# Kernel tuning notes

Hardware: AMD Instinct MI355X
Metric: run time of the kernel (lower is better)

## Reference

```python
import jax, jax.numpy as jnp
import numpy as np

S = 3      # SAMPLE_SIZE
U = 4      # UPSCALE
HID = 64


def _forward(x_in, sampler_w, sampler_b, w1, b1, w2, b2, w3, b3, w4, b4, w5, b5, w6, b6):
    B, C, H, W = x_in.shape  # C == 1
    Hp, Wp = H - (S - 1), W - (S - 1)
    # unfold: every 3x3 patch -> flattened vector of 9 (row-major i*3+j), matches F.unfold ordering
    img = x_in[:, 0]  # [B,H,W]
    patches = jnp.stack(
        [img[:, i:i + Hp, j:j + Wp] for i in range(S) for j in range(S)], axis=-1
    )  # [B,Hp,Wp,9]
    # AutoSample: softmax over the 9 taps per output channel, bias forced to zero
    wsamp = jax.nn.softmax(sampler_w.reshape(4, S * S), axis=1)  # [4,9]
    s = jnp.einsum('bhwk,ck->bhwc', patches, wsamp) + sampler_b * 0.0  # [B,Hp,Wp,4]
    # PixelShuffle(2) on [N,4,1,1] -> [N,1,2,2]: spatial (i,j) = channel i*2+j.
    # conv1 (2x2 kernel on 2x2 input) == dense over those 4 values; w1 is conv1.weight.reshape(64,4)
    x = jnp.einsum('bhwc,oc->bhwo', s, w1) + b1  # [B,Hp,Wp,64]
    # chain of 1x1 convs with ReLU before each
    for w, b in ((w2, b2), (w3, b3), (w4, b4), (w5, b5)):
        x = jnp.einsum('bhwi,oi->bhwo', jax.nn.relu(x), w) + b
    y = jnp.einsum('bhwi,oi->bhwo', jax.nn.relu(x), w6) + b6  # [B,Hp,Wp,16]
    # PixelShuffle(4) per patch + fold(stride=4): channel i*4+j -> output (h*4+i, w*4+j)
    y = y.reshape(B, Hp, Wp, U, U).transpose(0, 1, 3, 2, 4).reshape(B, 1, Hp * U, Wp * U)
    return y


def setup_inputs() -> dict:
    key = jax.random.key(0)
    ks = jax.random.split(key, 9)
    B, H, W = 16, 256, 256
    he4 = float(np.sqrt(2.0 / 4.0))
    he64 = float(np.sqrt(2.0 / 64.0))
    he9 = float(np.sqrt(2.0 / 9.0))
    return {
        'x_in': jax.random.normal(ks[0], (B, 1, H, W), jnp.float32),
        'sampler_w': jax.random.normal(ks[1], (4, 1, S, S), jnp.float32) * he9,
        'sampler_b': jnp.zeros((4,), jnp.float32),
        'w1': jax.random.normal(ks[2], (HID, 4), jnp.float32) * he4,
        'b1': jnp.zeros((HID,), jnp.float32),
        'w2': jax.random.normal(ks[3], (HID, HID), jnp.float32) * he64,
        'b2': jnp.zeros((HID,), jnp.float32),
        'w3': jax.random.normal(ks[4], (HID, HID), jnp.float32) * he64,
        'b3': jnp.zeros((HID,), jnp.float32),
        'w4': jax.random.normal(ks[5], (HID, HID), jnp.float32) * he64,
        'b4': jnp.zeros((HID,), jnp.float32),
        'w5': jax.random.normal(ks[6], (HID, HID), jnp.float32) * he64,
        'b5': jnp.zeros((HID,), jnp.float32),
        'w6': jax.random.normal(ks[7], (U * U, HID), jnp.float32) * he64,
        'b6': jnp.zeros((U * U,), jnp.float32),
    }


def reference(x_in, sampler_w, sampler_b, w1, b1, w2, b2, w3, b3, w4, b4, w5, b5, w6, b6):
    return _forward(x_in, sampler_w, sampler_b, w1, b1, w2, b2, w3, b3, w4, b4, w5, b5, w6, b6)
```

## Files before the change

### kernel.cpp

```cpp
#include <hip/hip_runtime.h>


typedef _Float16 f16x8  __attribute__((ext_vector_type(8)));
typedef _Float16 half2v __attribute__((ext_vector_type(2)));
typedef float    f32x16 __attribute__((ext_vector_type(16)));
typedef unsigned int u32;
typedef u32 u32x4 __attribute__((ext_vector_type(4)));

union FragU { f16x8 v; u32 w[4]; };

__device__ __forceinline__ u32 pkrne(float a, float b) {
    half2v h; h.x = (_Float16)a; h.y = (_Float16)b;
    return __builtin_bit_cast(u32, h);
}
__device__ __forceinline__ u32 pkrtz(float a, float b) {
    return __builtin_bit_cast(u32, __builtin_amdgcn_cvt_pkrtz(a, b));
}
__device__ __forceinline__ u32 pk_relu(u32 a) {
    half2v z = {};
    half2v r = __builtin_elementwise_max(__builtin_bit_cast(half2v, a), z);
    return __builtin_bit_cast(u32, r);
}

__device__ __forceinline__ f32x16 mfma16(const FragU& a, const FragU& b, f32x16 c) {
    return __builtin_amdgcn_mfma_f32_32x32x16_f16(a.v, b.v, c, 0, 0, 0);
}

__device__ __forceinline__ void pl32(u32& x, u32& y) {
    auto r = __builtin_amdgcn_permlane32_swap((int)x, (int)y, false, false);
    x = (u32)r[0]; y = (u32)r[1];
}

__device__ __forceinline__ void calc_coords(int g, int m, int& b, int& hp, int& wp) {
    unsigned P = (unsigned)(g * 32 + m);
    unsigned bb = P / 64516u;
    unsigned rem = P - bb * 64516u;
    unsigned h = rem / 254u;
    b = (int)bb; hp = (int)h; wp = (int)(rem - h * 254u);
}

__device__ __forceinline__ void prep_group(const float* __restrict__ x_in,
                                           int g, int m, int lo,
                                           float p[9], u32& ooff) {
    constexpr int OW = 1016;
    int b, hp, wp;
    calc_coords(g, m, b, hp, wp);
    const float* base = x_in + ((size_t)b << 16) + hp * 256 + wp;
#pragma unroll
    for (int i = 0; i < 3; ++i)
#pragma unroll
        for (int j = 0; j < 3; ++j)
            p[i * 3 + j] = base[i * 256 + j];
    ooff = (u32)b * (OW * OW) + (u32)(4 * hp + lo) * OW + 4 * wp;
}

__device__ __forceinline__ void init_bias(f32x16& a0, f32x16& a1,
                                          f32x16& b0, f32x16& b1v,
                                          const float* __restrict__ bb, int lo) {
#pragma unroll
    for (int mt = 0; mt < 2; ++mt) {
#pragma unroll
        for (int q = 0; q < 4; ++q) {
            const float4 t = *(const float4*)(bb + 32 * mt + 8 * q + 4 * lo);
            f32x16& A = mt ? a1 : a0;
            f32x16& B = mt ? b1v : b0;
            A[4 * q + 0] = t.x; A[4 * q + 1] = t.y;
            A[4 * q + 2] = t.z; A[4 * q + 3] = t.w;
            B[4 * q + 0] = t.x; B[4 * q + 1] = t.y;
            B[4 * q + 2] = t.z; B[4 * q + 3] = t.w;
        }
    }
}

__device__ __forceinline__ void epilogue(const f32x16& A0, const f32x16& A1,
                                         FragU (&B)[4]) {
    u32 ww[2][4][2];
#pragma unroll
    for (int mt = 0; mt < 2; ++mt) {
        const f32x16& A = mt ? A1 : A0;
#pragma unroll
        for (int q = 0; q < 4; ++q) {
            ww[mt][q][0] = pk_relu(pkrtz(A[4 * q + 0], A[4 * q + 1]));
            ww[mt][q][1] = pk_relu(pkrtz(A[4 * q + 2], A[4 * q + 3]));
        }
    }
#pragma unroll
    for (int ks = 0; ks < 4; ++ks) {
#pragma unroll
        for (int p = 0; p < 2; ++p) {
            u32 a = ww[ks >> 1][2 * (ks & 1) + 0][p];
            u32 b = ww[ks >> 1][2 * (ks & 1) + 1][p];
            pl32(a, b);
            B[ks].w[p]     = a;
            B[ks].w[p + 2] = b;
        }
    }
}

__device__ __forceinline__ void pack_B1(const float p[9], int lo, FragU& B1) {
    if (lo == 0) {
        B1.w[0] = pkrtz(p[0], p[1]);
        B1.w[1] = pkrtz(p[2], p[3]);
        B1.w[2] = pkrtz(p[4], p[5]);
        B1.w[3] = pkrtz(p[6], p[7]);
    } else {
        B1.w[0] = pkrtz(p[8], 0.0f);
        B1.w[1] = 0; B1.w[2] = 0; B1.w[3] = 0;
    }
}

__global__ __launch_bounds__(256, 1) void srnet_mfma(
    const float* __restrict__ x_in,
    const float* __restrict__ sampler_w,
    const float* __restrict__ w1, const float* __restrict__ b1,
    const float* __restrict__ w2, const float* __restrict__ b2,
    const float* __restrict__ w3, const float* __restrict__ b3,
    const float* __restrict__ w4, const float* __restrict__ b4,
    const float* __restrict__ w5, const float* __restrict__ b5,
    const float* __restrict__ w6, const float* __restrict__ b6,
    float* __restrict__ out)
{
    constexpr int NPAIR = 16129;
    constexpr int OW    = 1016;

    const int lane = threadIdx.x & 63;
    const int m    = lane & 31;
    const int lo   = lane >> 5;

    __shared__ u32x4 wlds[2048];
    __shared__ __align__(16) float bias_f32[336];

    const float* wptr[4] = { w2, w3, w4, w5 };
    for (int e = threadIdx.x; e < 2048; e += 256) {
        const int L  = e >> 9;
        const int f  = (e >> 6) & 7;
        const int l  = e & 63;
        const int mt = f >> 2, ks = f & 3;
        const float* src = wptr[L] + (32 * mt + (l & 31)) * 64 + 16 * ks + 8 * (l >> 5);
        const float4 f0 = *(const float4*)(src);
        const float4 f1 = *(const float4*)(src + 4);
        u32x4 v;
        v.x = pkrne(f0.x, f0.y); v.y = pkrne(f0.z, f0.w);
        v.z = pkrne(f1.x, f1.y); v.w = pkrne(f1.z, f1.w);
        wlds[e] = v;
    }
    for (int i = threadIdx.x; i < 336; i += 256) {
        float v;
        if      (i < 64)  v = b1[i];
        else if (i < 128) v = b2[i - 64];
        else if (i < 192) v = b3[i - 128];
        else if (i < 256) v = b4[i - 192];
        else if (i < 320) v = b5[i - 256];
        else              v = b6[i - 320];
        bias_f32[i] = v;
    }
    __syncthreads();

    float ws[4][9];
#pragma unroll
    for (int c = 0; c < 4; ++c) {
        float mx = sampler_w[c * 9];
#pragma unroll
        for (int k = 1; k < 9; ++k) mx = fmaxf(mx, sampler_w[c * 9 + k]);
        float e[9]; float sum = 0.f;
#pragma unroll
        for (int k = 0; k < 9; ++k) { e[k] = __expf(sampler_w[c * 9 + k] - mx); sum += e[k]; }
        float inv = 1.f / sum;
#pragma unroll
        for (int k = 0; k < 9; ++k) ws[c][k] = e[k] * inv;
    }

    FragU w1f[2];
#pragma unroll
    for (int mt = 0; mt < 2; ++mt) {
        const int row = 32 * mt + m;
        const float4 wr = *(const float4*)(w1 + row * 4);
        float we[9];
#pragma unroll
        for (int k = 0; k < 9; ++k)
            we[k] = wr.x * ws[0][k] + wr.y * ws[1][k] + wr.z * ws[2][k] + wr.w * ws[3][k];
        if (lo == 0) {
            w1f[mt].w[0] = pkrne(we[0], we[1]);
            w1f[mt].w[1] = pkrne(we[2], we[3]);
            w1f[mt].w[2] = pkrne(we[4], we[5]);
            w1f[mt].w[3] = pkrne(we[6], we[7]);
        } else {
            w1f[mt].w[0] = pkrne(we[8], 0.f);
            w1f[mt].w[1] = 0; w1f[mt].w[2] = 0; w1f[mt].w[3] = 0;
        }
    }

    FragU w6f[4];
    const bool vrow = (m < 16);
    const int r6 = vrow ? m : 0;
#pragma unroll
    for (int ks = 0; ks < 4; ++ks) {
        const float* src = w6 + r6 * 64 + 16 * ks + 8 * lo;
        const float4 f0 = *(const float4*)(src);
        const float4 f1 = *(const float4*)(src + 4);
        w6f[ks].w[0] = vrow ? pkrne(f0.x, f0.y) : 0;
        w6f[ks].w[1] = vrow ? pkrne(f0.z, f0.w) : 0;
        w6f[ks].w[2] = vrow ? pkrne(f1.x, f1.y) : 0;
        w6f[ks].w[3] = vrow ? pkrne(f1.z, f1.w) : 0;
    }

    const int wid = (int)((blockIdx.x * blockDim.x + threadIdx.x) >> 6);
    const int nw  = (int)((gridDim.x * blockDim.x) >> 6);

    int pg = wid;
    float pa[9], pb[9];
    u32 oa = 0, ob = 0;
    if (pg < NPAIR) {
        prep_group(x_in, 2 * pg + 0, m, lo, pa, oa);
        prep_group(x_in, 2 * pg + 1, m, lo, pb, ob);
    }

    while (pg < NPAIR) {
        const int pgn = pg + nw;

        FragU B1a, B1b;
        pack_B1(pa, lo, B1a);
        pack_B1(pb, lo, B1b);

        float na[9], nb[9];
        u32 noa = 0, nob = 0;
        if (pgn < NPAIR) {
            prep_group(x_in, 2 * pgn + 0, m, lo, na, noa);
            prep_group(x_in, 2 * pgn + 1, m, lo, nb, nob);
        }

        f32x16 aa0, aa1, ab0, ab1;
        init_bias(aa0, aa1, ab0, ab1, bias_f32 + 0, lo);
        aa0 = mfma16(w1f[0], B1a, aa0);
        ab0 = mfma16(w1f[0], B1b, ab0);
        aa1 = mfma16(w1f[1], B1a, aa1);
        ab1 = mfma16(w1f[1], B1b, ab1);

        FragU Ba[4], Bb[4];
        epilogue(aa0, aa1, Ba);
        epilogue(ab0, ab1, Bb);

#pragma unroll
        for (int L = 0; L < 4; ++L) {
            FragU Wf[8];
#pragma unroll
            for (int f = 0; f < 8; ++f) {
                u32x4 v = wlds[(L * 8 + f) * 64 + lane];
                Wf[f].w[0] = v.x; Wf[f].w[1] = v.y;
                Wf[f].w[2] = v.z; Wf[f].w[3] = v.w;
            }
            f32x16 ca0, ca1, cb0, cb1;
            init_bias(ca0, ca1, cb0, cb1, bias_f32 + 64 * (L + 1), lo);
#pragma unroll
            for (int ks = 0; ks < 4; ++ks) {
                ca0 = mfma16(Wf[ks],     Ba[ks], ca0);
                cb0 = mfma16(Wf[ks],     Bb[ks], cb0);
                ca1 = mfma16(Wf[4 + ks], Ba[ks], ca1);
                cb1 = mfma16(Wf[4 + ks], Bb[ks], cb1);
            }
            epilogue(ca0, ca1, Ba);
            epilogue(cb0, cb1, Bb);
        }

        f32x16 aFa, aFb;
        {
            const float4 t0 = *(const float4*)(bias_f32 + 320 + 4 * lo);
            const float4 t1 = *(const float4*)(bias_f32 + 320 + 8 + 4 * lo);
#pragma unroll
            for (int j = 0; j < 4; ++j) {
                aFa[j]      = ((const float*)&t0)[j];
                aFa[4 + j]  = ((const float*)&t1)[j];
                aFa[8 + j]  = 0.f;
                aFa[12 + j] = 0.f;
            }
            aFb = aFa;
        }
#pragma unroll
        for (int ks = 0; ks < 4; ++ks) {
            aFa = mfma16(w6f[ks], Ba[ks], aFa);
            aFb = mfma16(w6f[ks], Bb[ks], aFb);
        }

#pragma unroll
        for (int gi = 0; gi < 2; ++gi) {
            const f32x16& aF = gi ? aFb : aFa;
            float* obase = out + (gi ? ob : oa);
            *(float4*)(obase)          = make_float4(aF[0], aF[1], aF[2], aF[3]);
            *(float4*)(obase + 2 * OW) = make_float4(aF[4], aF[5], aF[6], aF[7]);
        }

        pg = pgn;
        oa = noa; ob = nob;
#pragma unroll
        for (int k = 0; k < 9; ++k) { pa[k] = na[k]; pb[k] = nb[k]; }
    }
}

extern "C" void kernel_launch(void* const* d_in, const int* in_sizes, int n_in,
                              void* d_out, int out_size, void* d_ws, size_t ws_size,
                              hipStream_t stream)
{
    const float* x_in      = (const float*)d_in[0];
    const float* sampler_w = (const float*)d_in[1];
    const float* w1 = (const float*)d_in[3];
    const float* b1 = (const float*)d_in[4];
    const float* w2 = (const float*)d_in[5];
    const float* b2 = (const float*)d_in[6];
    const float* w3 = (const float*)d_in[7];
    const float* b3 = (const float*)d_in[8];
    const float* w4 = (const float*)d_in[9];
    const float* b4 = (const float*)d_in[10];
    const float* w5 = (const float*)d_in[11];
    const float* b5 = (const float*)d_in[12];
    const float* w6 = (const float*)d_in[13];
    const float* b6 = (const float*)d_in[14];
    float* out = (float*)d_out;

    dim3 grid(512);
    dim3 block(256);
    hipLaunchKernelGGL(srnet_mfma, grid, block, 0, stream,
                       x_in, sampler_w, w1, b1, w2, b2, w3, b3,
                       w4, b4, w5, b5, w6, b6, out);
}
```

Before: 62.38 us.

## Move w1/w6 fragments to LDS, drop input prefetch, reuse accumulators

Precomputes the softmax-folded w1 fragments and the w6 fragments once per block into shared memory, instead of having every thread keep them in registers. The layer weights are now loaded from LDS one k-slice at a time rather than all eight fragments at once. The software prefetch of the next patch group is removed and the accumulators are reused across layers. This is meant to cut register pressure, but it exposes global load latency that the prefetch used to hide and adds LDS traffic.

```diff
diff --git a/kernel.cpp b/kernel.cpp
--- a/kernel.cpp
+++ b/kernel.cpp
@@ -107,6 +107,14 @@
         B1.w[0] = pkrtz(p[8], 0.0f);
         B1.w[1] = 0; B1.w[2] = 0; B1.w[3] = 0;
     }
+}
+
+__device__ __forceinline__ FragU lds_frag(const u32x4* __restrict__ wlds,
+                                          int slot, int lane) {
+    u32x4 v = wlds[slot * 64 + lane];
+    FragU f;
+    f.w[0] = v.x; f.w[1] = v.y; f.w[2] = v.z; f.w[3] = v.w;
+    return f;
 }
 
 __global__ __launch_bounds__(256, 1) void srnet_mfma(
@@ -127,7 +135,7 @@
     const int m    = lane & 31;
     const int lo   = lane >> 5;
 
-    __shared__ u32x4 wlds[2048];
+    __shared__ u32x4 wlds[38 * 64];
     __shared__ __align__(16) float bias_f32[336];
 
     const float* wptr[4] = { w2, w3, w4, w5 };
@@ -142,7 +150,55 @@
         u32x4 v;
         v.x = pkrne(f0.x, f0.y); v.y = pkrne(f0.z, f0.w);
         v.z = pkrne(f1.x, f1.y); v.w = pkrne(f1.z, f1.w);
-        wlds[e] = v;
+        wlds[(2 + L * 8 + f) * 64 + l] = v;
+    }
+    if (threadIdx.x < 64) {
+        const int l = threadIdx.x, lm = l & 31, llo = l >> 5;
+        const bool vr = (lm < 16);
+        const int r6 = vr ? lm : 0;
+#pragma unroll
+        for (int ks = 0; ks < 4; ++ks) {
+            const float* src = w6 + r6 * 64 + 16 * ks + 8 * llo;
+            const float4 f0 = *(const float4*)(src);
+            const float4 f1 = *(const float4*)(src + 4);
+            u32x4 v;
+            v.x = vr ? pkrne(f0.x, f0.y) : 0; v.y = vr ? pkrne(f0.z, f0.w) : 0;
+            v.z = vr ? pkrne(f1.x, f1.y) : 0; v.w = vr ? pkrne(f1.z, f1.w) : 0;
+            wlds[(34 + ks) * 64 + l] = v;
+        }
+    }
+    if (threadIdx.x >= 64 && threadIdx.x < 128) {
+        const int l = threadIdx.x - 64, lm = l & 31, llo = l >> 5;
+        float ws[4][9];
+#pragma unroll
+        for (int c = 0; c < 4; ++c) {
+            float mx = sampler_w[c * 9];
+#pragma unroll
+            for (int k = 1; k < 9; ++k) mx = fmaxf(mx, sampler_w[c * 9 + k]);
+            float e[9]; float sum = 0.f;
+#pragma unroll
+            for (int k = 0; k < 9; ++k) { e[k] = __expf(sampler_w[c * 9 + k] - mx); sum += e[k]; }
+            float inv = 1.f / sum;
+#pragma unroll
+            for (int k = 0; k < 9; ++k) ws[c][k] = e[k] * inv;
+        }
+#pragma unroll
+        for (int mt = 0; mt < 2; ++mt) {
+            const int row = 32 * mt + lm;
+            const float4 wr = *(const float4*)(w1 + row * 4);
+            float we[9];
+#pragma unroll
+            for (int k = 0; k < 9; ++k)
+                we[k] = wr.x * ws[0][k] + wr.y * ws[1][k] + wr.z * ws[2][k] + wr.w * ws[3][k];
+            u32x4 v;
+            if (llo == 0) {
+                v.x = pkrne(we[0], we[1]); v.y = pkrne(we[2], we[3]);
+                v.z = pkrne(we[4], we[5]); v.w = pkrne(we[6], we[7]);
+            } else {
+                v.x = pkrne(we[8], 0.f); v.y = 0; v.z = 0; v.w = 0;
+            }
+            wlds[mt * 64 + l] = v;
+        }
     }
     for (int i = threadIdx.x; i < 336; i += 256) {
         float v;
@@ -156,143 +212,78 @@
     }
     __syncthreads();
 
-    float ws[4][9];
-#pragma unroll
-    for (int c = 0; c < 4; ++c) {
-        float mx = sampler_w[c * 9];
-#pragma unroll
-        for (int k = 1; k < 9; ++k) mx = fmaxf(mx, sampler_w[c * 9 + k]);
-        float e[9]; float sum = 0.f;
-#pragma unroll
-        for (int k = 0; k < 9; ++k) { e[k] = __expf(sampler_w[c * 9 + k] - mx); sum += e[k]; }
-        float inv = 1.f / sum;
-#pragma unroll
-        for (int k = 0; k < 9; ++k) ws[c][k] = e[k] * inv;
-    }
-
-    FragU w1f[2];
-#pragma unroll
-    for (int mt = 0; mt < 2; ++mt) {
-        const int row = 32 * mt + m;
-        const float4 wr = *(const float4*)(w1 + row * 4);
-        float we[9];
-#pragma unroll
-        for (int k = 0; k < 9; ++k)
-            we[k] = wr.x * ws[0][k] + wr.y * ws[1][k] + wr.z * ws[2][k] + wr.w * ws[3][k];
-        if (lo == 0) {
-            w1f[mt].w[0] = pkrne(we[0], we[1]);
-            w1f[mt].w[1] = pkrne(we[2], we[3]);
-            w1f[mt].w[2] = pkrne(we[4], we[5]);
-            w1f[mt].w[3] = pkrne(we[6], we[7]);
-        } else {
-            w1f[mt].w[0] = pkrne(we[8], 0.f);
-            w1f[mt].w[1] = 0; w1f[mt].w[2] = 0; w1f[mt].w[3] = 0;
-        }
-    }
-
-    FragU w6f[4];
-    const bool vrow = (m < 16);
-    const int r6 = vrow ? m : 0;
-#pragma unroll
-    for (int ks = 0; ks < 4; ++ks) {
-        const float* src = w6 + r6 * 64 + 16 * ks + 8 * lo;
-        const float4 f0 = *(const float4*)(src);
-        const float4 f1 = *(const float4*)(src + 4);
-        w6f[ks].w[0] = vrow ? pkrne(f0.x, f0.y) : 0;
-        w6f[ks].w[1] = vrow ? pkrne(f0.z, f0.w) : 0;
-        w6f[ks].w[2] = vrow ? pkrne(f1.x, f1.y) : 0;
-        w6f[ks].w[3] = vrow ? pkrne(f1.z, f1.w) : 0;
-    }
-
     const int wid = (int)((blockIdx.x * blockDim.x + threadIdx.x) >> 6);
     const int nw  = (int)((gridDim.x * blockDim.x) >> 6);
 
-    int pg = wid;
-    float pa[9], pb[9];
-    u32 oa = 0, ob = 0;
-    if (pg < NPAIR) {
+    for (int pg = wid; pg < NPAIR; pg += nw) {
+        float pa[9], pb[9];
+        u32 oa, ob;
         prep_group(x_in, 2 * pg + 0, m, lo, pa, oa);
         prep_group(x_in, 2 * pg + 1, m, lo, pb, ob);
-    }
-
-    while (pg < NPAIR) {
-        const int pgn = pg + nw;
 
         FragU B1a, B1b;
         pack_B1(pa, lo, B1a);
         pack_B1(pb, lo, B1b);
 
-        float na[9], nb[9];
-        u32 noa = 0, nob = 0;
-        if (pgn < NPAIR) {
-            prep_group(x_in, 2 * pgn + 0, m, lo, na, noa);
-            prep_group(x_in, 2 * pgn + 1, m, lo, nb, nob);
-        }
-
-        f32x16 aa0, aa1, ab0, ab1;
-        init_bias(aa0, aa1, ab0, ab1, bias_f32 + 0, lo);
-        aa0 = mfma16(w1f[0], B1a, aa0);
-        ab0 = mfma16(w1f[0], B1b, ab0);
-        aa1 = mfma16(w1f[1], B1a, aa1);
-        ab1 = mfma16(w1f[1], B1b, ab1);
+        f32x16 c0a, c1a, c0b, c1b;
+
+        init_bias(c0a, c1a, c0b, c1b, bias_f32 + 0, lo);
+        {
+            FragU wA = lds_frag(wlds, 0, lane);
+            FragU wB = lds_frag(wlds, 1, lane);
+            c0a = mfma16(wA, B1a, c0a);
+            c0b = mfma16(wA, B1b, c0b);
+            c1a = mfma16(wB, B1a, c1a);
+            c1b = mfma16(wB, B1b, c1b);
+        }
 
         FragU Ba[4], Bb[4];
-        epilogue(aa0, aa1, Ba);
-        epilogue(ab0, ab1, Bb);
+        epilogue(c0a, c1a, Ba);
+        epilogue(c0b, c1b, Bb);
 
 #pragma unroll
         for (int L = 0; L < 4; ++L) {
-            FragU Wf[8];
-#pragma unroll
-            for (int f = 0; f < 8; ++f) {
-                u32x4 v = wlds[(L * 8 + f) * 64 + lane];
-                Wf[f].w[0] = v.x; Wf[f].w[1] = v.y;
-                Wf[f].w[2] = v.z; Wf[f].w[3] = v.w;
+            init_bias(c0a, c1a, c0b, c1b, bias_f32 + 64 * (L + 1), lo);
+#pragma unroll
+            for (int ks = 0; ks < 4; ++ks) {
+                FragU w0 = lds_frag(wlds, 2 + L * 8 + ks,     lane);
+                FragU w1l = lds_frag(wlds, 2 + L * 8 + 4 + ks, lane);
+                c0a = mfma16(w0,  Ba[ks], c0a);
+                c0b = mfma16(w0,  Bb[ks], c0b);
+                c1a = mfma16(w1l, Ba[ks], c1a);
+                c1b = mfma16(w1l, Bb[ks], c1b);
             }
-            f32x16 ca0, ca1, cb0, cb1;
-            init_bias(ca0, ca1, cb0, cb1, bias_f32 + 64 * (L + 1), lo);
-#pragma unroll
-            for (int ks = 0; ks < 4; ++ks) {
-                ca0 = mfma16(Wf[ks],     Ba[ks], ca0);
-                cb0 = mfma16(Wf[ks],     Bb[ks], cb0);
-                ca1 = mfma16(Wf[4 + ks], Ba[ks], ca1);
-                cb1 = mfma16(Wf[4 + ks], Bb[ks], cb1);
-            }
-            epilogue(ca0, ca1, Ba);
-            epilogue(cb0, cb1, Bb);
-        }
-
-        f32x16 aFa, aFb;
+            epilogue(c0a, c1a, Ba);
+            epilogue(c0b, c1b, Bb);
+        }
+
         {
             const float4 t0 = *(const float4*)(bias_f32 + 320 + 4 * lo);
             const float4 t1 = *(const float4*)(bias_f32 + 320 + 8 + 4 * lo);
 #pragma unroll
             for (int j = 0; j < 4; ++j) {
-                aFa[j]      = ((const float*)&t0)[j];
-                aFa[4 + j]  = ((const float*)&t1)[j];
-                aFa[8 + j]  = 0.f;
-                aFa[12 + j] = 0.f;
+                c0a[j]      = ((const float*)&t0)[j];
+                c0a[4 + j]  = ((const float*)&t1)[j];
+                c0a[8 + j]  = 0.f;
+                c0a[12 + j] = 0.f;
             }
-            aFb = aFa;
+            c0b = c0a;
         }
 #pragma unroll
         for (int ks = 0; ks < 4; ++ks) {
-            aFa = mfma16(w6f[ks], Ba[ks], aFa);
-            aFb = mfma16(w6f[ks], Bb[ks], aFb);
-        }
-
-#pragma unroll
-        for (int gi = 0; gi < 2; ++gi) {
-            const f32x16& aF = gi ? aFb : aFa;
-            float* obase = out + (gi ? ob : oa);
-            *(float4*)(obase)          = make_float4(aF[0], aF[1], aF[2], aF[3]);
-            *(float4*)(obase + 2 * OW) = make_float4(aF[4], aF[5], aF[6], aF[7]);
-        }
-
-        pg = pgn;
-        oa = noa; ob = nob;
-#pragma unroll
-        for (int k = 0; k < 9; ++k) { pa[k] = na[k]; pb[k] = nb[k]; }
+            FragU w6f = lds_frag(wlds, 34 + ks, lane);
+            c0a = mfma16(w6f, Ba[ks], c0a);
+            c0b = mfma16(w6f, Bb[ks], c0b);
+        }
+
+        {
+            float* obase = out + oa;
+            *(float4*)(obase)          = make_float4(c0a[0], c0a[1], c0a[2], c0a[3]);
+            *(float4*)(obase + 2 * OW) = make_float4(c0a[4], c0a[5], c0a[6], c0a[7]);
+            obase = out + ob;
+            *(float4*)(obase)          = make_float4(c0b[0], c0b[1], c0b[2], c0b[3]);
+            *(float4*)(obase + 2 * OW) = make_float4(c0b[4], c0b[5], c0b[6], c0b[7]);
+        }
     }
 }
 
```

New measurement: 64.66 us. +3.7%, slower.
